# Optimization experiments

Hardware: AMD Instinct MI355X
Metric: run time of the kernel (lower is better)

## Reference

```python
import jax, jax.numpy as jnp
import numpy as np

B, IN, H = 16384, 128, 512
NH = 4
HD = H // NH


def setup_inputs() -> dict:
    key = jax.random.key(0)
    ks = jax.random.split(key, 20)
    s = lambda k, shape: jax.random.normal(k, shape, dtype=jnp.float32) * 0.05
    return {
        "x": jax.random.normal(ks[0], (B, IN), dtype=jnp.float32),
        "hidden_left": jax.random.normal(ks[1], (B, H), dtype=jnp.float32),
        "hidden_up": jax.random.normal(ks[2], (B, H), dtype=jnp.float32),
        "hidden_prev": jax.random.normal(ks[3], (B, H), dtype=jnp.float32),
        # input_proj
        "W_in": s(ks[4], (H, IN)),
        "b_in": jnp.zeros((H,), jnp.float32),
        # MultiheadAttention (packed qkv in-proj + out-proj), torch convention W:[out,in]
        "attn_in_w": s(ks[5], (3 * H, H)),
        "attn_in_b": jnp.zeros((3 * H,), jnp.float32),
        "attn_out_w": s(ks[6], (H, H)),
        "attn_out_b": jnp.zeros((H,), jnp.float32),
        # spatial_gate: Linear(3H -> H) then sigmoid
        "W_gate": s(ks[7], (H, 3 * H)),
        "b_gate": jnp.zeros((H,), jnp.float32),
        # GRUCell (torch layout: [3H, .] with r,z,n blocks)
        "gru_w_ih": s(ks[8], (3 * H, IN)),
        "gru_w_hh": s(ks[9], (3 * H, H)),
        "gru_b_ih": jnp.zeros((3 * H,), jnp.float32),
        "gru_b_hh": jnp.zeros((3 * H,), jnp.float32),
    }


def reference(x, hidden_left, hidden_up, hidden_prev,
              W_in, b_in, attn_in_w, attn_in_b, attn_out_w, attn_out_b,
              W_gate, b_gate, gru_w_ih, gru_w_hh, gru_b_ih, gru_b_hh):
    # input projection
    x_proj = x @ W_in.T + b_in  # [B, H]

    # spatial attention over the 2 neighbor states
    sp = jnp.stack([hidden_left, hidden_up], axis=1)          # [B, 2, H]
    qkv = sp @ attn_in_w.T + attn_in_b                        # [B, 2, 3H]
    q, k, v = jnp.split(qkv, 3, axis=-1)
    q = q.reshape(-1, 2, NH, HD)
    k = k.reshape(-1, 2, NH, HD)
    v = v.reshape(-1, 2, NH, HD)
    scores = jnp.einsum("bqhd,bkhd->bhqk", q, k) / jnp.sqrt(jnp.float32(HD))
    attn = jax.nn.softmax(scores, axis=-1)                    # [B, NH, 2, 2]
    ctx = jnp.einsum("bhqk,bkhd->bqhd", attn, v).reshape(-1, 2, H)
    sp_out = ctx @ attn_out_w.T + attn_out_b                  # [B, 2, H]
    spatial_combined = sp_out.mean(axis=1)                    # [B, H]

    # gated blend into previous hidden
    gate_in = jnp.concatenate([hidden_prev, spatial_combined, x_proj], axis=1)
    gate = jax.nn.sigmoid(gate_in @ W_gate.T + b_gate)
    enhanced_prev = hidden_prev + gate * spatial_combined

    # GRUCell(x, enhanced_prev), torch gate order r, z, n
    gi = x @ gru_w_ih.T + gru_b_ih                            # [B, 3H]
    gh = enhanced_prev @ gru_w_hh.T + gru_b_hh                # [B, 3H]
    i_r, i_z, i_n = jnp.split(gi, 3, axis=1)
    h_r, h_z, h_n = jnp.split(gh, 3, axis=1)
    r = jax.nn.sigmoid(i_r + h_r)
    z = jax.nn.sigmoid(i_z + h_z)
    n = jnp.tanh(i_n + r * h_n)
    new_hidden = (1.0 - z) * n + z * enhanced_prev
    # dropout is identity in eval mode
    return new_hidden
```

## Files before the change

kernel.cpp:

```cpp
#include <hip/hip_runtime.h>
#include <hip/hip_bf16.h>
#include <stdint.h>


#define NB 16384

typedef __attribute__((ext_vector_type(8))) __bf16 bf16x8;
typedef __attribute__((ext_vector_type(4))) float f32x4;
typedef __attribute__((ext_vector_type(8))) unsigned short u16x8;

__device__ __forceinline__ unsigned short f2bf(float f) {
  union { float f; unsigned int u; } v; v.f = f;
  unsigned int u = v.u;
  unsigned int r = (u + 0x7fffu + ((u >> 16) & 1u)) >> 16;
  return (unsigned short)r;
}
__device__ __forceinline__ float bf2f(unsigned short h) {
  union { unsigned int u; float f; } v; v.u = ((unsigned int)h) << 16;
  return v.f;
}
__device__ __forceinline__ float sigmoidf_(float x) {
  return 1.0f / (1.0f + __expf(-x));
}

#define J0 (512 * 128 / 8)
#define J1 (1536 * 128 / 8)
#define J2 (1536 * 512 / 8)
#define J3 (512 * 512 / 8)
#define J4 (512 * 1536 / 8)
#define J5 (1536 * 512 / 8)
#define J6 (NB * 128 / 8)
#define J7 (NB * 512 / 8)
#define J8 (NB * 512 / 8)
#define J9 (NB * 512 / 8)
#define C1 (J0)
#define C2 (C1 + J1)
#define C3 (C2 + J2)
#define C4 (C3 + J3)
#define C5 (C4 + J4)
#define C6 (C5 + J5)
#define C7 (C6 + J6)
#define C8 (C7 + J7)
#define C9 (C8 + J8)
#define CT (C9 + J9)

struct CvtJobs {
  const float* src[10];
  unsigned short* dst[10];
};

__global__ void cvt_multi(CvtJobs j) {
  int g = blockIdx.x * blockDim.x + threadIdx.x;
  if (g >= CT) return;
  int k, base;
  if (g < C4) {
    if (g < C2) {
      if (g < C1) { k = 0; base = 0; } else { k = 1; base = C1; }
    } else {
      if (g < C3) { k = 2; base = C2; } else { k = 3; base = C3; }
    }
  } else {
    if (g < C6) {
      if (g < C5) { k = 4; base = C4; } else { k = 5; base = C5; }
    } else {
      if (g < C7) { k = 6; base = C6; }
      else if (g < C8) { k = 7; base = C7; }
      else if (g < C9) { k = 8; base = C8; }
      else { k = 9; base = C9; }
    }
  }
  int local = g - base;
  const float4* s = (const float4*)j.src[k] + (size_t)local * 2;
  float4 a = s[0], b = s[1];
  u16x8 o;
  o[0] = f2bf(a.x); o[1] = f2bf(a.y); o[2] = f2bf(a.z); o[3] = f2bf(a.w);
  o[4] = f2bf(b.x); o[5] = f2bf(b.y); o[6] = f2bf(b.z); o[7] = f2bf(b.w);
  size_t didx;
  if (k == 7)      didx = ((size_t)(local >> 6) << 7) + (local & 63);
  else if (k == 8) didx = ((size_t)(local >> 6) << 7) + 64 + (local & 63);
  else if (k == 9) didx = (size_t)(local >> 6) * 192 + (local & 63);
  else             didx = (size_t)local;
  *((u16x8*)j.dst[k] + didx) = o;
}

__device__ __forceinline__ void gl_lds16(const unsigned short* g, unsigned short* l) {
  __builtin_amdgcn_global_load_lds(
      (const __attribute__((address_space(1))) void*)g,
      (__attribute__((address_space(3))) void*)l, 16, 0, 0);
}

template <int EPI>
__global__ __launch_bounds__(512, 1) void gemm_big(
    const unsigned short* __restrict__ A, int lda,
    const unsigned short* __restrict__ W, int ldw,
    const float* __restrict__ bias, const float* __restrict__ bias2,
    int K, int ntx,
    unsigned short* __restrict__ outb, int ldob,
    unsigned short* __restrict__ outb2, int ldob2) {
  __shared__ unsigned short lds[65536];
  unsigned short* Asb = lds;
  unsigned short* Bsb = lds + 32768;
  const int tid = threadIdx.x;
  const int lane = tid & 63;
  const int wave = tid >> 6;

  const int nwg = gridDim.x;
  const int cpx = nwg >> 3;
  const int bid = blockIdx.x;
  const int id = (bid & 7) * cpx + (bid >> 3);
  const int bx = id % ntx;
  const int by = id / ntx;

  const int m0 = by * 256;
  const int n0 = bx * 256;
  const int ar0 = (wave >> 2) * 64;
  const int br0 = (wave & 3) * 32;

  f32x4 acc[4][4][2] = {};

  const int srow = tid >> 3;
  const int presw = (tid & 7) ^ (srow & 7);
  const unsigned short* Ag = A + (size_t)(m0 + srow) * lda + presw * 8;
  const unsigned short* Wg = W + (size_t)(n0 + srow) * ldw + presw * 8;
  unsigned short* Asd = Asb + tid * 8;
  unsigned short* Wsd = Bsb + tid * 8;

  auto stageA = [&](int buf, int h, int k0) {
    const unsigned short* s = Ag + (size_t)(h * 128) * lda + k0;
    unsigned short* d = Asd + buf * 16384 + h * 8192;
    gl_lds16(s, d);
    gl_lds16(s + (size_t)64 * lda, d + 4096);
  };
  auto stageB = [&](int buf, int h, int k0) {
    const unsigned short* s = Wg + (size_t)(h * 128) * ldw + k0;
    unsigned short* d = Wsd + buf * 16384 + h * 8192;
    gl_lds16(s, d);
    gl_lds16(s + (size_t)64 * ldw, d + 4096);
  };

  const int lrow = lane & 15;
  const int kq = (lane >> 4) * 8;
  const int sw = (lrow & 7) << 3;
  const int NT = K >> 6;

  stageA(0, 0, 0);
  stageB(0, 0, 0);
  stageB(0, 1, 0);
  stageA(0, 1, 0);
  asm volatile("s_waitcnt vmcnt(4)" ::: "memory");
  __builtin_amdgcn_s_barrier();

  bf16x8 a[4][2], b0[2][2], b1[2][2];

#define RD_A(X, H)                                                            \
  _Pragma("unroll") for (int m = 0; m < 4; ++m)                               \
  _Pragma("unroll") for (int kk = 0; kk < 2; ++kk)                            \
      a[m][kk] = *(const bf16x8*)&Asb[(X) * 16384 +                           \
                                      ((H) * 128 + ar0 + m * 16 + lrow) * 64 +\
                                      ((kk * 32 + kq) ^ sw)];
#define RD_B(X, H, DST)                                                       \
  _Pragma("unroll") for (int n = 0; n < 2; ++n)                               \
  _Pragma("unroll") for (int kk = 0; kk < 2; ++kk)                            \
      DST[n][kk] = *(const bf16x8*)&Bsb[(X) * 16384 +                         \
                                        ((H) * 128 + br0 + n * 16 + lrow) * 64 + \
                                        ((kk * 32 + kq) ^ sw)];
#define MFMA_Q(Q, BF)                                                         \
  __builtin_amdgcn_s_setprio(1);                                              \
  _Pragma("unroll") for (int m = 0; m < 4; ++m)                               \
  _Pragma("unroll") for (int n = 0; n < 2; ++n)                               \
  _Pragma("unroll") for (int kk = 0; kk < 2; ++kk)                            \
      acc[Q][m][n] = __builtin_amdgcn_mfma_f32_16x16x32_bf16(                 \
          a[m][kk], BF[n][kk], acc[Q][m][n], 0, 0, 0);                        \
  __builtin_amdgcn_s_setprio(0);
#define LGKM0                                                                 \
  asm volatile("s_waitcnt lgkmcnt(0)" ::: "memory");                          \
  __builtin_amdgcn_sched_barrier(0);
#define BAR __builtin_amdgcn_s_barrier();

  for (int t = 0; t < NT - 1; ++t) {
    const int X = t & 1, Y = X ^ 1;
    const int kn = (t + 1) << 6;
    RD_A(X, 0)
    RD_B(X, 0, b0)
    stageA(Y, 0, kn);
    stageB(Y, 0, kn);
    asm volatile("s_waitcnt vmcnt(4)" ::: "memory");
    BAR LGKM0
    MFMA_Q(0, b0)
    BAR
    RD_B(X, 1, b1)
    stageB(Y, 1, kn);
    BAR LGKM0
    MFMA_Q(1, b1)
    BAR
    RD_A(X, 1)
    stageA(Y, 1, kn);
    BAR LGKM0
    MFMA_Q(2, b1)
    BAR
    asm volatile("s_waitcnt vmcnt(4)" ::: "memory");
    BAR
    __builtin_amdgcn_sched_barrier(0);
    MFMA_Q(3, b0)
    BAR
  }
  {
    const int X = (NT - 1) & 1;
    RD_A(X, 0)
    RD_B(X, 0, b0)
    asm volatile("s_waitcnt vmcnt(0)" ::: "memory");
    BAR LGKM0
    MFMA_Q(0, b0)
    RD_B(X, 1, b1)
    LGKM0
    MFMA_Q(1, b1)
    RD_A(X, 1)
    LGKM0
    MFMA_Q(2, b1)
    MFMA_Q(3, b0)
  }
#undef RD_A
#undef RD_B
#undef MFMA_Q
#undef LGKM0
#undef BAR

  __syncthreads();
  unsigned short* ob = outb;
  int ld = ldob, ncof = n0;
  const float* bp = bias;
  if constexpr (EPI == 2) {
    if (n0 >= 512) { ob = outb2; ld = ldob2; ncof = n0 - 512; bp = bias2; }
  }
  const int qr[4] = {0, 0, 128, 128};
  const int qc[4] = {0, 128, 128, 0};
  const int ri = (lane >> 4) << 2;
#pragma unroll
  for (int q = 0; q < 4; ++q) {
#pragma unroll
    for (int n = 0; n < 2; ++n) {
      const int col = qc[q] + br0 + n * 16 + lrow;
      const float bv = bp ? bp[ncof + col] : 0.0f;
      const int g8 = col >> 3, c7 = col & 7;
#pragma unroll
      for (int m = 0; m < 4; ++m)
#pragma unroll
        for (int i = 0; i < 4; ++i) {
          const int row = qr[q] + ar0 + m * 16 + ri + i;
          lds[row * 256 + ((g8 ^ (row & 7)) << 3) + c7] =
              f2bf(acc[q][m][n][i] + bv);
        }
    }
  }
  __syncthreads();
#pragma unroll
  for (int jj = 0; jj < 16; ++jj) {
    int c = jj * 512 + tid;
    int row = c >> 5;
    int slot = c & 31;
    u16x8 v = *(const u16x8*)&lds[row * 256 + ((slot ^ (row & 7)) << 3)];
    *(u16x8*)&ob[(size_t)(m0 + row) * ld + ncof + slot * 8] = v;
  }
}

__global__ __launch_bounds__(512, 1) void qkva(
    const unsigned short* __restrict__ A,
    const unsigned short* __restrict__ W,
    const float* __restrict__ bias,
    unsigned short* __restrict__ ctx) {
  __shared__ unsigned short lds[65536];
  unsigned short* Asb = lds;
  unsigned short* Bsb = lds + 16384;
  const int tid = threadIdx.x;
  const int lane = tid & 63;
  const int wave = tid >> 6;

  const int nwg = gridDim.x;
  const int cpx = nwg >> 3;
  const int bid = blockIdx.x;
  const int id = (bid & 7) * cpx + (bid >> 3);
  const int bx = id & 3;
  const int by = id >> 2;

  const int m0 = by * 128;
  const int h0 = bx * 128;
  const int wm = (wave >> 2) * 64;
  const int wj = (wave & 3) * 32;

  f32x4 acc[4][6] = {};

  const int srow = tid >> 3;
  const int presw = (tid & 7) ^ (srow & 7);
  const unsigned short* Ag = A + (size_t)(m0 + srow) * 512 + presw * 8;
  unsigned short* Asd = Asb + tid * 8;
  unsigned short* Bsd = Bsb + tid * 8;

  auto stage = [&](int buf, int k0) {
    gl_lds16(Ag + k0, Asd + buf * 8192);
    gl_lds16(Ag + (size_t)64 * 512 + k0, Asd + buf * 8192 + 4096);
#pragma unroll
    for (int l = 0; l < 6; ++l) {
      const int gate = l >> 1;
      const int rr = (l & 1) * 64 + srow;
      gl_lds16(W + (size_t)(gate * 512 + h0 + rr) * 512 + presw * 8 + k0,
               Bsd + buf * 24576 + l * 4096);
    }
  };

  stage(0, 0);
  int cur = 0;
  const int lrow = lane & 15;
  const int kq = (lane >> 4) * 8;
  const int sw = (lrow & 7) << 3;

  for (int k0 = 0; k0 < 512; k0 += 64) {
    if (k0 + 64 < 512) {
      stage(cur ^ 1, k0 + 64);
      asm volatile("s_waitcnt vmcnt(8)" ::: "memory");
    } else {
      asm volatile("s_waitcnt vmcnt(0)" ::: "memory");
    }
    __builtin_amdgcn_s_barrier();
    const unsigned short* Ab = Asb + cur * 8192;
    const unsigned short* Bb = Bsb + cur * 24576;
    bf16x8 a[4][2], b[6][2];
#pragma unroll
    for (int m = 0; m < 4; ++m)
#pragma unroll
      for (int kk = 0; kk < 2; ++kk)
        a[m][kk] = *(const bf16x8*)&Ab[(wm + m * 16 + lrow) * 64 +
                                       ((kk * 32 + kq) ^ sw)];
#pragma unroll
    for (int f = 0; f < 6; ++f)
#pragma unroll
      for (int kk = 0; kk < 2; ++kk) {
        const int brow = (f >> 1) * 128 + wj + (f & 1) * 16 + lrow;
        b[f][kk] = *(const bf16x8*)&Bb[brow * 64 + ((kk * 32 + kq) ^ sw)];
      }
    __builtin_amdgcn_s_setprio(1);
#pragma unroll
    for (int m = 0; m < 4; ++m)
#pragma unroll
      for (int f = 0; f < 6; ++f)
#pragma unroll
        for (int kk = 0; kk < 2; ++kk)
          acc[m][f] = __builtin_amdgcn_mfma_f32_16x16x32_bf16(a[m][kk], b[f][kk],
                                                              acc[m][f], 0, 0, 0);
    __builtin_amdgcn_s_setprio(0);
    __builtin_amdgcn_s_barrier();
    cur ^= 1;
  }

  __syncthreads();
  const int ri = (lane >> 4) << 2;
#pragma unroll
  for (int f = 0; f < 6; ++f) {
    const int gate = f >> 1;
    const int col = wj + (f & 1) * 16 + lrow;
    const float bv = bias[gate * 512 + h0 + col];
#pragma unroll
    for (int m = 0; m < 4; ++m)
#pragma unroll
      for (int i = 0; i < 4; ++i) {
        const int row = wm + m * 16 + ri + i;
        lds[gate * 17408 + row * 136 + col] = f2bf(acc[m][f][i] + bv);
      }
  }
  __syncthreads();

  const int l = tid & 15;
  const int grp = tid >> 4;
#pragma unroll
  for (int it = 0; it < 2; ++it) {
    const int p = it * 32 + grp;
    const int r0 = 2 * p, r1 = 2 * p + 1;
    u16x8 q0 = *(const u16x8*)&lds[r0 * 136 + l * 8];
    u16x8 q1 = *(const u16x8*)&lds[r1 * 136 + l * 8];
    u16x8 k0 = *(const u16x8*)&lds[17408 + r0 * 136 + l * 8];
    u16x8 k1 = *(const u16x8*)&lds[17408 + r1 * 136 + l * 8];
    u16x8 v0 = *(const u16x8*)&lds[34816 + r0 * 136 + l * 8];
    u16x8 v1 = *(const u16x8*)&lds[34816 + r1 * 136 + l * 8];
    float s00 = 0.f, s01 = 0.f, s10 = 0.f, s11 = 0.f;
    float v0f[8], v1f[8];
#pragma unroll
    for (int i = 0; i < 8; ++i) {
      float q0f = bf2f(q0[i]), q1f = bf2f(q1[i]);
      float k0f = bf2f(k0[i]), k1f = bf2f(k1[i]);
      v0f[i] = bf2f(v0[i]); v1f[i] = bf2f(v1[i]);
      s00 += q0f * k0f; s01 += q0f * k1f;
      s10 += q1f * k0f; s11 += q1f * k1f;
    }
#pragma unroll
    for (int off = 1; off < 16; off <<= 1) {
      s00 += __shfl_xor(s00, off);
      s01 += __shfl_xor(s01, off);
      s10 += __shfl_xor(s10, off);
      s11 += __shfl_xor(s11, off);
    }
    const float scale = 0.0883883476483184f;
    s00 *= scale; s01 *= scale; s10 *= scale; s11 *= scale;
    float mx0 = fmaxf(s00, s01), mx1 = fmaxf(s10, s11);
    float a00 = __expf(s00 - mx0), a01 = __expf(s01 - mx0);
    float a10 = __expf(s10 - mx1), a11 = __expf(s11 - mx1);
    float c0 = 0.5f * (a00 / (a00 + a01) + a10 / (a10 + a11));
    float c1 = 0.5f * (a01 / (a00 + a01) + a11 / (a10 + a11));
    u16x8 o;
#pragma unroll
    for (int i = 0; i < 8; ++i) o[i] = f2bf(c0 * v0f[i] + c1 * v1f[i]);
    const int bglob = (m0 >> 1) + p;
    *(u16x8*)&ctx[(size_t)bglob * 512 + h0 + l * 8] = o;
  }
}

__global__ __launch_bounds__(512, 1) void g7_gru(
    const unsigned short* __restrict__ A, int lda,
    const unsigned short* __restrict__ W, int ldw,
    const float* __restrict__ b_hh, int K, int ntx,
    const unsigned short* __restrict__ gi,
    const unsigned short* __restrict__ enh,
    float* __restrict__ out) {
  __shared__ unsigned short lds[65536];
  unsigned short* Asb = lds;
  unsigned short* Bsb = lds + 16384;
  const int tid = threadIdx.x;
  const int lane = tid & 63;
  const int wave = tid >> 6;

  const int nwg = gridDim.x;
  const int cpx = nwg >> 3;
  const int bid = blockIdx.x;
  const int id = (bid & 7) * cpx + (bid >> 3);
  const int bx = id % ntx;
  const int by = id / ntx;

  const int m0 = by * 128;
  const int j0 = bx * 128;
  const int wm = (wave >> 2) * 64;
  const int wj = (wave & 3) * 32;

  f32x4 acc[4][6] = {};

  const int srow = tid >> 3;
  const int presw = (tid & 7) ^ (srow & 7);
  const unsigned short* Ag = A + (size_t)(m0 + srow) * lda + presw * 8;
  unsigned short* Asd = Asb + tid * 8;
  unsigned short* Bsd = Bsb + tid * 8;

  auto stage = [&](int buf, int k0) {
    gl_lds16(Ag + k0, Asd + buf * 8192);
    gl_lds16(Ag + (size_t)64 * lda + k0, Asd + buf * 8192 + 4096);
#pragma unroll
    for (int l = 0; l < 6; ++l) {
      const int gate = l >> 1;
      const int rr = (l & 1) * 64 + srow;
      gl_lds16(W + (size_t)(gate * 512 + j0 + rr) * ldw + presw * 8 + k0,
               Bsd + buf * 24576 + l * 4096);
    }
  };

  stage(0, 0);
  int cur = 0;
  const int lrow = lane & 15;
  const int kq = (lane >> 4) * 8;
  const int sw = (lrow & 7) << 3;

  for (int k0 = 0; k0 < K; k0 += 64) {
    if (k0 + 64 < K) {
      stage(cur ^ 1, k0 + 64);
      asm volatile("s_waitcnt vmcnt(8)" ::: "memory");
    } else {
      asm volatile("s_waitcnt vmcnt(0)" ::: "memory");
    }
    __builtin_amdgcn_s_barrier();
    const unsigned short* Ab = Asb + cur * 8192;
    const unsigned short* Bb = Bsb + cur * 24576;
    bf16x8 a[4][2], b[6][2];
#pragma unroll
    for (int m = 0; m < 4; ++m)
#pragma unroll
      for (int kk = 0; kk < 2; ++kk)
        a[m][kk] = *(const bf16x8*)&Ab[(wm + m * 16 + lrow) * 64 +
                                       ((kk * 32 + kq) ^ sw)];
#pragma unroll
    for (int f = 0; f < 6; ++f)
#pragma unroll
      for (int kk = 0; kk < 2; ++kk) {
        const int brow = (f >> 1) * 128 + wj + (f & 1) * 16 + lrow;
        b[f][kk] = *(const bf16x8*)&Bb[brow * 64 + ((kk * 32 + kq) ^ sw)];
      }
    __builtin_amdgcn_s_setprio(1);
#pragma unroll
    for (int m = 0; m < 4; ++m)
#pragma unroll
      for (int f = 0; f < 6; ++f)
#pragma unroll
        for (int kk = 0; kk < 2; ++kk)
          acc[m][f] = __builtin_amdgcn_mfma_f32_16x16x32_bf16(a[m][kk], b[f][kk],
                                                              acc[m][f], 0, 0, 0);
    __builtin_amdgcn_s_setprio(0);
    __builtin_amdgcn_s_barrier();
    cur ^= 1;
  }

  __syncthreads();
  const int ri = (lane >> 4) << 2;
#pragma unroll
  for (int f = 0; f < 6; ++f) {
    const int gate = f >> 1;
    const int col = wj + (f & 1) * 16 + lrow;
    const float bh = b_hh[gate * 512 + j0 + col];
#pragma unroll
    for (int m = 0; m < 4; ++m)
#pragma unroll
      for (int i = 0; i < 4; ++i) {
        const int row = wm + m * 16 + ri + i;
        lds[gate * 17408 + row * 136 + col] = f2bf(acc[m][f][i] + bh);
      }
  }
  __syncthreads();

#pragma unroll
  for (int cc = 0; cc < 4; ++cc) {
    const int c = cc * 512 + tid;
    const int row = c >> 4, slot = c & 15;
    const int rg = m0 + row;
    const int jb = j0 + slot * 8;
    u16x8 hr = *(const u16x8*)&lds[row * 136 + slot * 8];
    u16x8 hz = *(const u16x8*)&lds[17408 + row * 136 + slot * 8];
    u16x8 hn = *(const u16x8*)&lds[34816 + row * 136 + slot * 8];
    const size_t gb = (size_t)rg * 1536 + jb;
    u16x8 ir = *(const u16x8*)&gi[gb];
    u16x8 iz = *(const u16x8*)&gi[gb + 512];
    u16x8 in_ = *(const u16x8*)&gi[gb + 1024];
    u16x8 ev = *(const u16x8*)&enh[(size_t)rg * 512 + jb];
    float of[8];
#pragma unroll
    for (int i = 0; i < 8; ++i) {
      float rr = sigmoidf_(bf2f(ir[i]) + bf2f(hr[i]));
      float zz = sigmoidf_(bf2f(iz[i]) + bf2f(hz[i]));
      float nn = tanhf(bf2f(in_[i]) + rr * bf2f(hn[i]));
      of[i] = (1.0f - zz) * nn + zz * bf2f(ev[i]);
    }
    float* op = out + (size_t)rg * 512 + jb;
    *(float4*)op = make_float4(of[0], of[1], of[2], of[3]);
    *(float4*)(op + 4) = make_float4(of[4], of[5], of[6], of[7]);
  }
}

template <int EPI>
__global__ __launch_bounds__(256, 2) void gemm_bt(
    const unsigned short* __restrict__ A, int lda,
    const unsigned short* __restrict__ W, int ldw,
    const float* __restrict__ bias, int K, int ntx,
    unsigned short* __restrict__ outb, int ldob,
    const unsigned short* __restrict__ gin) {
  __shared__ unsigned short As[2][128 * 64];
  __shared__ unsigned short Ws[2][128 * 64];
  const int tid = threadIdx.x;
  const int lane = tid & 63;
  const int wave = tid >> 6;

  const int nwg = gridDim.x;
  const int cpx = nwg >> 3;
  const int bid = blockIdx.x;
  const int id = (bid & 7) * cpx + (bid >> 3);
  const int bx = id % ntx;
  const int by = id / ntx;

  const int m0 = by * 128;
  const int n0 = bx * 128;
  const int wm = (wave >> 1) * 64;
  const int wn = (wave & 1) * 64;

  f32x4 acc[4][4] = {};

  const int srow = tid >> 3;
  const int sslot = (tid & 7) ^ (srow & 7);
  const unsigned short* Ag = A + (size_t)(m0 + srow) * lda + sslot * 8;
  const unsigned short* Wg = W + (size_t)(n0 + srow) * ldw + sslot * 8;
  unsigned short* Asd = &As[0][tid * 8];
  unsigned short* Wsd = &Ws[0][tid * 8];

  auto stage = [&](int buf, int k0) {
#pragma unroll
    for (int i = 0; i < 4; ++i) {
      gl_lds16(Ag + (size_t)(i * 32) * lda + k0, Asd + buf * 8192 + i * 2048);
      gl_lds16(Wg + (size_t)(i * 32) * ldw + k0, Wsd + buf * 8192 + i * 2048);
    }
  };

  stage(0, 0);
  int cur = 0;
  const int lrow = lane & 15;
  const int kq = (lane >> 4) * 8;
  const int sw = (lrow & 7) << 3;

  for (int k0 = 0; k0 < K; k0 += 64) {
    if (k0 + 64 < K) {
      stage(cur ^ 1, k0 + 64);
      asm volatile("s_waitcnt vmcnt(8)" ::: "memory");
    } else {
      asm volatile("s_waitcnt vmcnt(0)" ::: "memory");
    }
    __builtin_amdgcn_s_barrier();
#pragma unroll
    for (int kk = 0; kk < 2; ++kk) {
      const int kr = kk * 32 + kq;
      const int ki = kr ^ sw;
      bf16x8 af[4], wf[4];
#pragma unroll
      for (int m = 0; m < 4; ++m)
        af[m] = *(const bf16x8*)&As[cur][(wm + m * 16 + lrow) * 64 + ki];
#pragma unroll
      for (int n = 0; n < 4; ++n)
        wf[n] = *(const bf16x8*)&Ws[cur][(wn + n * 16 + lrow) * 64 + ki];
#pragma unroll
      for (int m = 0; m < 4; ++m)
#pragma unroll
        for (int n = 0; n < 4; ++n)
          acc[m][n] = __builtin_amdgcn_mfma_f32_16x16x32_bf16(af[m], wf[n],
                                                              acc[m][n], 0, 0, 0);
    }
    __builtin_amdgcn_s_barrier();
    cur ^= 1;
  }

  unsigned short* Cs = &As[0][0];
  const int r0l = wm + ((lane >> 4) << 2);
  const int c0l = wn + lrow;
  if constexpr (EPI == 1) {
#pragma unroll
    for (int n = 0; n < 4; ++n) {
      const int col = c0l + n * 16;
      const float bv = bias ? bias[n0 + col] : 0.0f;
#pragma unroll
      for (int m = 0; m < 4; ++m)
#pragma unroll
        for (int i = 0; i < 4; ++i)
          Cs[(r0l + m * 16 + i) * 128 + col] =
              f2bf(sigmoidf_(acc[m][n][i] + bv));
    }
    __syncthreads();
#pragma unroll
    for (int q = 0; q < 8; ++q) {
      const int c = q * 256 + tid;
      const int row = c >> 4, slot = c & 15;
      const int rg = m0 + row;
      const int cb = n0 + slot * 8;
      u16x8 gv = *(const u16x8*)&Cs[row * 128 + slot * 8];
      const size_t rb = (size_t)rg * 1536 + cb;
      u16x8 hpv = *(const u16x8*)&gin[rb];
      u16x8 scv = *(const u16x8*)&gin[rb + 512];
      u16x8 o;
#pragma unroll
      for (int i = 0; i < 8; ++i)
        o[i] = f2bf(bf2f(hpv[i]) + bf2f(gv[i]) * bf2f(scv[i]));
      *(u16x8*)&outb[(size_t)rg * 512 + cb] = o;
    }
  } else {
#pragma unroll
    for (int n = 0; n < 4; ++n) {
      const int col = c0l + n * 16;
      const float bv = bias ? bias[n0 + col] : 0.0f;
#pragma unroll
      for (int m = 0; m < 4; ++m)
#pragma unroll
        for (int i = 0; i < 4; ++i)
          Cs[(r0l + m * 16 + i) * 128 + col] = f2bf(acc[m][n][i] + bv);
    }
    __syncthreads();
#pragma unroll
    for (int jj = 0; jj < 8; ++jj) {
      int c = jj * 256 + tid;
      int row = c >> 4;
      int slot = c & 15;
      u16x8 v = *(const u16x8*)&Cs[row * 128 + slot * 8];
      *(u16x8*)&outb[(size_t)(m0 + row) * ldob + n0 + slot * 8] = v;
    }
  }
}

extern "C" void kernel_launch(void* const* d_in, const int* in_sizes, int n_in,
                              void* d_out, int out_size, void* d_ws, size_t ws_size,
                              hipStream_t stream) {
  const float* x = (const float*)d_in[0];
  const float* hl = (const float*)d_in[1];
  const float* hu = (const float*)d_in[2];
  const float* hp = (const float*)d_in[3];
  const float* W_in = (const float*)d_in[4];
  const float* b_in = (const float*)d_in[5];
  const float* attn_in_w = (const float*)d_in[6];
  const float* attn_in_b = (const float*)d_in[7];
  const float* attn_out_w = (const float*)d_in[8];
  const float* attn_out_b = (const float*)d_in[9];
  const float* W_gate = (const float*)d_in[10];
  const float* b_gate = (const float*)d_in[11];
  const float* gru_w_ih = (const float*)d_in[12];
  const float* gru_w_hh = (const float*)d_in[13];
  const float* gru_b_ih = (const float*)d_in[14];
  const float* gru_b_hh = (const float*)d_in[15];

  char* ws = (char*)d_ws;
  size_t off = 0;
  auto alloc = [&](size_t bytes) {
    void* p = ws + off;
    off += (bytes + 255) & ~(size_t)255;
    return p;
  };
  unsigned short* wComb = (unsigned short*)alloc((size_t)2048 * 128 * 2);
  unsigned short* wAin  = (unsigned short*)alloc((size_t)1536 * 512 * 2);
  unsigned short* wAout = (unsigned short*)alloc((size_t)512 * 512 * 2);
  unsigned short* wGate = (unsigned short*)alloc((size_t)512 * 1536 * 2);
  unsigned short* wHh   = (unsigned short*)alloc((size_t)1536 * 512 * 2);
  unsigned short* xb   = (unsigned short*)alloc((size_t)NB * 128 * 2);
  unsigned short* hlib = (unsigned short*)alloc((size_t)2 * NB * 512 * 2);
  unsigned short* gate_in = (unsigned short*)alloc((size_t)NB * 1536 * 2);
  unsigned short* qkvb = (unsigned short*)alloc((size_t)2 * NB * 1536 * 2);
  unsigned short* ctxb = (unsigned short*)alloc((size_t)NB * 512 * 2);
  unsigned short* enhb = (unsigned short*)alloc((size_t)NB * 512 * 2);
  unsigned short* gi = qkvb;

  (void)ws_size; (void)in_sizes; (void)n_in; (void)out_size;

  const int T = 256;

  CvtJobs jobs;
  jobs.src[0] = W_in;       jobs.dst[0] = wComb;
  jobs.src[1] = gru_w_ih;   jobs.dst[1] = wComb + (size_t)512 * 128;
  jobs.src[2] = attn_in_w;  jobs.dst[2] = wAin;
  jobs.src[3] = attn_out_w; jobs.dst[3] = wAout;
  jobs.src[4] = W_gate;     jobs.dst[4] = wGate;
  jobs.src[5] = gru_w_hh;   jobs.dst[5] = wHh;
  jobs.src[6] = x;          jobs.dst[6] = xb;
  jobs.src[7] = hl;         jobs.dst[7] = hlib;
  jobs.src[8] = hu;         jobs.dst[8] = hlib;
  jobs.src[9] = hp;         jobs.dst[9] = gate_in;
  cvt_multi<<<(CT + T - 1) / T, T, 0, stream>>>(jobs);

  const int MTB = NB / 256;
  const int MTS = NB / 128;

  qkva<<<1024, dim3(512), 0, stream>>>(hlib, wAin, attn_in_b, ctxb);
  gemm_bt<0><<<4 * MTS, T, 0, stream>>>(ctxb, 512, wAout, 512, attn_out_b,
                                        512, 4,
                                        gate_in + 512, 1536, nullptr);
  gemm_big<2><<<8 * MTB, dim3(512), 0, stream>>>(xb, 128, wComb, 128,
                                                 b_in, gru_b_ih, 128, 8,
                                                 gate_in + 1024, 1536, gi, 1536);
  gemm_bt<1><<<4 * MTS, T, 0, stream>>>(gate_in, 1536, wGate, 1536, b_gate,
                                        1536, 4,
                                        enhb, 512, gate_in);
  g7_gru<<<4 * MTS, dim3(512), 0, stream>>>(enhb, 512, wHh, 512, gru_b_hh,
                                            512, 4, gi, enhb, (float*)d_out);
}
```

Measured before the change: 221.6 us.

## Replace 128x128 GEMM kernel with 128x256-tile 512-thread wide GEMM for out-proj and gate

Swaps the 256-thread 128x128-tile gemm_bt used for the attention out-projection and the spatial-gate GEMM for a new 512-thread kernel with 128x256 tiles. Each A tile is now reused across twice as many output columns, which halves the number of workgroups and the A-operand global traffic. The new kernel also raises wave priority around the MFMA block and uses a swizzled LDS epilogue for the stores. In exchange, occupancy drops to one workgroup per CU and the grid is smaller, which can reduce latency hiding.

```diff
diff --git a/kernel.cpp b/kernel.cpp
--- a/kernel.cpp
+++ b/kernel.cpp
@@ -263,6 +263,129 @@
   }
 }
 
+template <int EPI>
+__global__ __launch_bounds__(512, 1) void gemm_wide(
+    const unsigned short* __restrict__ A, int lda,
+    const unsigned short* __restrict__ W, int ldw,
+    const float* __restrict__ bias, int K, int ntx,
+    unsigned short* __restrict__ outb, int ldob,
+    const unsigned short* __restrict__ gin) {
+  __shared__ unsigned short lds[49152];
+  unsigned short* Asb = lds;
+  unsigned short* Bsb = lds + 16384;
+  const int tid = threadIdx.x;
+  const int lane = tid & 63;
+  const int wave = tid >> 6;
+
+  const int nwg = gridDim.x;
+  const int cpx = nwg >> 3;
+  const int bid = blockIdx.x;
+  const int id = (bid & 7) * cpx + (bid >> 3);
+  const int bx = id % ntx;
+  const int by = id / ntx;
+
+  const int m0 = by * 128;
+  const int n0 = bx * 256;
+  const int wm = (wave >> 2) * 64;
+  const int wn = (wave & 3) * 64;
+
+  f32x4 acc[4][4] = {};
+
+  const int srow = tid >> 3;
+  const int presw = (tid & 7) ^ (srow & 7);
+  const unsigned short* Ag = A + (size_t)(m0 + srow) * lda + presw * 8;
+  const unsigned short* Wg = W + (size_t)(n0 + srow) * ldw + presw * 8;
+  unsigned short* Asd = Asb + tid * 8;
+  unsigned short* Bsd = Bsb + tid * 8;
+
+  auto stage = [&](int buf, int k0) {
+    gl_lds16(Ag + k0, Asd + buf * 8192);
+    gl_lds16(Ag + (size_t)64 * lda + k0, Asd + buf * 8192 + 4096);
+#pragma unroll
+    for (int l = 0; l < 4; ++l)
+      gl_lds16(Wg + (size_t)(l * 64) * ldw + k0, Bsd + buf * 16384 + l * 4096);
+  };
+
+  stage(0, 0);
+  int cur = 0;
+  const int lrow = lane & 15;
+  const int kq = (lane >> 4) * 8;
+  const int sw = (lrow & 7) << 3;
+
+  for (int k0 = 0; k0 < K; k0 += 64) {
+    if (k0 + 64 < K) {
+      stage(cur ^ 1, k0 + 64);
+      asm volatile("s_waitcnt vmcnt(6)" ::: "memory");
+    } else {
+      asm volatile("s_waitcnt vmcnt(0)" ::: "memory");
+    }
+    __builtin_amdgcn_s_barrier();
+    const unsigned short* Ab = Asb + cur * 8192;
+    const unsigned short* Bb = Bsb + cur * 16384;
+#pragma unroll
+    for (int kk = 0; kk < 2; ++kk) {
+      const int ki = (kk * 32 + kq) ^ sw;
+      bf16x8 af[4], wf[4];
+#pragma unroll
+      for (int m = 0; m < 4; ++m)
+        af[m] = *(const bf16x8*)&Ab[(wm + m * 16 + lrow) * 64 + ki];
+#pragma unroll
+      for (int n = 0; n < 4; ++n)
+        wf[n] = *(const bf16x8*)&Bb[(wn + n * 16 + lrow) * 64 + ki];
+      __builtin_amdgcn_s_setprio(1);
+#pragma unroll
+      for (int m = 0; m < 4; ++m)
+#pragma unroll
+        for (int n = 0; n < 4; ++n)
+          acc[m][n] = __builtin_amdgcn_mfma_f32_16x16x32_bf16(af[m], wf[n],
+                                                              acc[m][n], 0, 0, 0);
+      __builtin_amdgcn_s_setprio(0);
+    }
+    __builtin_amdgcn_s_barrier();
+    cur ^= 1;
+  }
+
+  __syncthreads();
+  const int ri = (lane >> 4) << 2;
+#pragma unroll
+  for (int n = 0; n < 4; ++n) {
+    const int col = wn + n * 16 + lrow;
+    const float bv = bias ? bias[n0 + col] : 0.0f;
+    const int g8 = col >> 3, c7 = col & 7;
+#pragma unroll
+    for (int m = 0; m < 4; ++m)
+#pragma unroll
+      for (int i = 0; i < 4; ++i) {
+        const int row = wm + m * 16 + ri + i;
+        float v = acc[m][n][i] + bv;
+        if constexpr (EPI == 1) v = sigmoidf_(v);
+        lds[row * 256 + ((g8 ^ (row & 7)) << 3) + c7] = f2bf(v);
+      }
+  }
+  __syncthreads();
+#pragma unroll
+  for (int jj = 0; jj < 8; ++jj) {
+    const int c = jj * 512 + tid;
+    const int row = c >> 5;
+    const int slot = c & 31;
+    u16x8 v = *(const u16x8*)&lds[row * 256 + ((slot ^ (row & 7)) << 3)];
+    if constexpr (EPI == 1) {
+      const int rg = m0 + row;
+      const int cb = n0 + slot * 8;
+      const size_t rb = (size_t)rg * 1536 + cb;
+      u16x8 hpv = *(const u16x8*)&gin[rb];
+      u16x8 scv = *(const u16x8*)&gin[rb + 512];
+      u16x8 o;
+#pragma unroll
+      for (int i = 0; i < 8; ++i)
+        o[i] = f2bf(bf2f(hpv[i]) + bf2f(v[i]) * bf2f(scv[i]));
+      *(u16x8*)&outb[(size_t)rg * 512 + cb] = o;
+    } else {
+      *(u16x8*)&outb[(size_t)(m0 + row) * ldob + n0 + slot * 8] = v;
+    }
+  }
+}
+
 __global__ __launch_bounds__(512, 1) void qkva(
     const unsigned short* __restrict__ A,
     const unsigned short* __restrict__ W,
@@ -544,139 +667,6 @@
     float* op = out + (size_t)rg * 512 + jb;
     *(float4*)op = make_float4(of[0], of[1], of[2], of[3]);
     *(float4*)(op + 4) = make_float4(of[4], of[5], of[6], of[7]);
-  }
-}
-
-template <int EPI>
-__global__ __launch_bounds__(256, 2) void gemm_bt(
-    const unsigned short* __restrict__ A, int lda,
-    const unsigned short* __restrict__ W, int ldw,
-    const float* __restrict__ bias, int K, int ntx,
-    unsigned short* __restrict__ outb, int ldob,
-    const unsigned short* __restrict__ gin) {
-  __shared__ unsigned short As[2][128 * 64];
-  __shared__ unsigned short Ws[2][128 * 64];
-  const int tid = threadIdx.x;
-  const int lane = tid & 63;
-  const int wave = tid >> 6;
-
-  const int nwg = gridDim.x;
-  const int cpx = nwg >> 3;
-  const int bid = blockIdx.x;
-  const int id = (bid & 7) * cpx + (bid >> 3);
-  const int bx = id % ntx;
-  const int by = id / ntx;
-
-  const int m0 = by * 128;
-  const int n0 = bx * 128;
-  const int wm = (wave >> 1) * 64;
-  const int wn = (wave & 1) * 64;
-
-  f32x4 acc[4][4] = {};
-
-  const int srow = tid >> 3;
-  const int sslot = (tid & 7) ^ (srow & 7);
-  const unsigned short* Ag = A + (size_t)(m0 + srow) * lda + sslot * 8;
-  const unsigned short* Wg = W + (size_t)(n0 + srow) * ldw + sslot * 8;
-  unsigned short* Asd = &As[0][tid * 8];
-  unsigned short* Wsd = &Ws[0][tid * 8];
-
-  auto stage = [&](int buf, int k0) {
-#pragma unroll
-    for (int i = 0; i < 4; ++i) {
-      gl_lds16(Ag + (size_t)(i * 32) * lda + k0, Asd + buf * 8192 + i * 2048);
-      gl_lds16(Wg + (size_t)(i * 32) * ldw + k0, Wsd + buf * 8192 + i * 2048);
-    }
-  };
-
-  stage(0, 0);
-  int cur = 0;
-  const int lrow = lane & 15;
-  const int kq = (lane >> 4) * 8;
-  const int sw = (lrow & 7) << 3;
-
-  for (int k0 = 0; k0 < K; k0 += 64) {
-    if (k0 + 64 < K) {
-      stage(cur ^ 1, k0 + 64);
-      asm volatile("s_waitcnt vmcnt(8)" ::: "memory");
-    } else {
-      asm volatile("s_waitcnt vmcnt(0)" ::: "memory");
-    }
-    __builtin_amdgcn_s_barrier();
-#pragma unroll
-    for (int kk = 0; kk < 2; ++kk) {
-      const int kr = kk * 32 + kq;
-      const int ki = kr ^ sw;
-      bf16x8 af[4], wf[4];
-#pragma unroll
-      for (int m = 0; m < 4; ++m)
-        af[m] = *(const bf16x8*)&As[cur][(wm + m * 16 + lrow) * 64 + ki];
-#pragma unroll
-      for (int n = 0; n < 4; ++n)
-        wf[n] = *(const bf16x8*)&Ws[cur][(wn + n * 16 + lrow) * 64 + ki];
-#pragma unroll
-      for (int m = 0; m < 4; ++m)
-#pragma unroll
-        for (int n = 0; n < 4; ++n)
-          acc[m][n] = __builtin_amdgcn_mfma_f32_16x16x32_bf16(af[m], wf[n],
-                                                              acc[m][n], 0, 0, 0);
-    }
-    __builtin_amdgcn_s_barrier();
-    cur ^= 1;
-  }
-
-  unsigned short* Cs = &As[0][0];
-  const int r0l = wm + ((lane >> 4) << 2);
-  const int c0l = wn + lrow;
-  if constexpr (EPI == 1) {
-#pragma unroll
-    for (int n = 0; n < 4; ++n) {
-      const int col = c0l + n * 16;
-      const float bv = bias ? bias[n0 + col] : 0.0f;
-#pragma unroll
-      for (int m = 0; m < 4; ++m)
-#pragma unroll
-        for (int i = 0; i < 4; ++i)
-          Cs[(r0l + m * 16 + i) * 128 + col] =
-              f2bf(sigmoidf_(acc[m][n][i] + bv));
-    }
-    __syncthreads();
-#pragma unroll
-    for (int q = 0; q < 8; ++q) {
-      const int c = q * 256 + tid;
-      const int row = c >> 4, slot = c & 15;
-      const int rg = m0 + row;
-      const int cb = n0 + slot * 8;
-      u16x8 gv = *(const u16x8*)&Cs[row * 128 + slot * 8];
-      const size_t rb = (size_t)rg * 1536 + cb;
-      u16x8 hpv = *(const u16x8*)&gin[rb];
-      u16x8 scv = *(const u16x8*)&gin[rb + 512];
-      u16x8 o;
-#pragma unroll
-      for (int i = 0; i < 8; ++i)
-        o[i] = f2bf(bf2f(hpv[i]) + bf2f(gv[i]) * bf2f(scv[i]));
-      *(u16x8*)&outb[(size_t)rg * 512 + cb] = o;
-    }
-  } else {
-#pragma unroll
-    for (int n = 0; n < 4; ++n) {
-      const int col = c0l + n * 16;
-      const float bv = bias ? bias[n0 + col] : 0.0f;
-#pragma unroll
-      for (int m = 0; m < 4; ++m)
-#pragma unroll
-        for (int i = 0; i < 4; ++i)
-          Cs[(r0l + m * 16 + i) * 128 + col] = f2bf(acc[m][n][i] + bv);
-    }
-    __syncthreads();
-#pragma unroll
-    for (int jj = 0; jj < 8; ++jj) {
-      int c = jj * 256 + tid;
-      int row = c >> 4;
-      int slot = c & 15;
-      u16x8 v = *(const u16x8*)&Cs[row * 128 + slot * 8];
-      *(u16x8*)&outb[(size_t)(m0 + row) * ldob + n0 + slot * 8] = v;
-    }
   }
 }
 
@@ -741,15 +731,15 @@
   const int MTS = NB / 128;
 
   qkva<<<1024, dim3(512), 0, stream>>>(hlib, wAin, attn_in_b, ctxb);
-  gemm_bt<0><<<4 * MTS, T, 0, stream>>>(ctxb, 512, wAout, 512, attn_out_b,
-                                        512, 4,
-                                        gate_in + 512, 1536, nullptr);
+  gemm_wide<0><<<2 * MTS, dim3(512), 0, stream>>>(ctxb, 512, wAout, 512,
+                                                  attn_out_b, 512, 2,
+                                                  gate_in + 512, 1536, nullptr);
   gemm_big<2><<<8 * MTB, dim3(512), 0, stream>>>(xb, 128, wComb, 128,
                                                  b_in, gru_b_ih, 128, 8,
                                                  gate_in + 1024, 1536, gi, 1536);
-  gemm_bt<1><<<4 * MTS, T, 0, stream>>>(gate_in, 1536, wGate, 1536, b_gate,
-                                        1536, 4,
-                                        enhb, 512, gate_in);
+  gemm_wide<1><<<2 * MTS, dim3(512), 0, stream>>>(gate_in, 1536, wGate, 1536,
+                                                  b_gate, 1536, 2,
+                                                  enhb, 512, gate_in);
   g7_gru<<<4 * MTS, dim3(512), 0, stream>>>(enhb, 512, wHh, 512, gru_b_hh,
                                             512, 4, gi, enhb, (float*)d_out);
 }
```

Measured after the change: 225.1 us. About the same (+1.6%).
